# Kernel optimization log

Hardware: AMD Instinct MI355X
Metric: run time of the kernel (lower is better)

## Reference

```python
import jax, jax.numpy as jnp
import numpy as np

N_RES = 320
C_Z = 128
NUM_HEAD = 4
HEAD_DIM = C_Z // NUM_HEAD  # 32
LN_EPS = 1e-5


def layer_norm(x, scale, offset):
    mean = jnp.mean(x, axis=-1, keepdims=True)
    var = jnp.var(x, axis=-1, keepdims=True)
    return (x - mean) * jax.lax.rsqrt(var + LN_EPS) * scale + offset


def setup_inputs() -> dict:
    key = jax.random.key(0)
    ks = jax.random.split(key, 12)
    d = {
        'pair_act': jax.random.normal(ks[0], (N_RES, N_RES, C_Z), jnp.float32),
        'affine_act': jax.random.normal(ks[1], (N_RES, N_RES, C_Z), jnp.float32),
        'pair_mask': jnp.ones((N_RES, N_RES), jnp.float32),
        'pair_ln_scale': jnp.ones((C_Z,), jnp.float32),
        'pair_ln_offset': jnp.zeros((C_Z,), jnp.float32),
        'affine_ln_scale': jnp.ones((C_Z,), jnp.float32),
        'affine_ln_offset': jnp.zeros((C_Z,), jnp.float32),
        'feat_2d_weights': jax.random.normal(ks[2], (C_Z, NUM_HEAD), jnp.float32) / 0.8796256610342398,
        'query_w': jax.random.normal(ks[3], (C_Z, NUM_HEAD, HEAD_DIM), jnp.float32) * 0.05,
        'key_w': jax.random.normal(ks[4], (C_Z, NUM_HEAD, HEAD_DIM), jnp.float32) * 0.05,
        'value_w': jax.random.normal(ks[5], (C_Z, NUM_HEAD, HEAD_DIM), jnp.float32) * 0.05,
        'gating_w': jax.random.normal(ks[6], (C_Z, NUM_HEAD, HEAD_DIM), jnp.float32) * 0.05,
        'output_w': jax.random.normal(ks[7], (NUM_HEAD, HEAD_DIM, C_Z), jnp.float32) * 0.05,
    }
    return d


def reference(pair_act, affine_act, pair_mask,
              pair_ln_scale, pair_ln_offset, affine_ln_scale, affine_ln_offset,
              feat_2d_weights, query_w, key_w, value_w, gating_w, output_w):
    # orientation == 'per_row' -> no swapaxes
    pair_ln = layer_norm(pair_act, pair_ln_scale, pair_ln_offset)          # [N,N,c]
    affine_ln = layer_norm(affine_act, affine_ln_scale, affine_ln_offset)  # [N,N,c]

    # padding bias [N,1,1,N]
    bias = (1e9 * (pair_mask - 1.0))[:, None, None, :]
    # nonbatched pair bias [H,N,N]
    nonbatched_bias = jnp.einsum('qkc,ch->hqk', affine_ln, feat_2d_weights)

    # attention (q_data == m_data == pair_ln)
    scale = HEAD_DIM ** (-0.5)
    q = jnp.einsum('bqa,ahc->bqhc', pair_ln, query_w) * scale
    k = jnp.einsum('bka,ahc->bkhc', pair_ln, key_w)
    v = jnp.einsum('bka,ahc->bkhc', pair_ln, value_w)

    logits = jnp.einsum('bqhc,bkhc->bhqk', q, k) + bias + nonbatched_bias[None]
    weights = jax.nn.softmax(logits, axis=-1)
    weighted_avg = jnp.einsum('bhqk,bkhc->bqhc', weights, v)

    gate = jax.nn.sigmoid(jnp.einsum('bqc,chv->bqhv', pair_ln, gating_w))
    weighted_avg = weighted_avg * gate

    out = jnp.einsum('bqhc,hco->bqo', weighted_avg, output_w)  # [N,N,c_z]
    return out
```

## Files before the change

### kernel.cpp

```cpp
#include <hip/hip_runtime.h>
#include <hip/hip_bf16.h>

#define N_RES 320
#define C_Z   128
#define NH    4
#define HD    32
#define M_TOT (N_RES*N_RES)
#define LN_EPS 1e-5f
#define QSCALE 0.17677669529663687f

typedef __attribute__((ext_vector_type(8))) short short8;
typedef __attribute__((ext_vector_type(4))) float floatx4;

typedef const __hip_bfloat16* bfp;

__device__ __forceinline__ float lo_bits(unsigned u){
    union { unsigned u; float f; } v; v.u = u << 16; return v.f;
}
__device__ __forceinline__ float hi_bits(unsigned u){
    union { unsigned u; float f; } v; v.u = u & 0xffff0000u; return v.f;
}
__device__ __forceinline__ float u16_to_f(unsigned short s){
    union { unsigned u; float f; } v; v.u = ((unsigned)s) << 16; return v.f;
}
__device__ __forceinline__ unsigned short bf16r(float f){
    union { __hip_bfloat16 b; unsigned short s; } v; v.b = __float2bfloat16(f); return v.s;
}
__device__ __forceinline__ unsigned pack2(float a, float b){
    return (unsigned)bf16r(a) | ((unsigned)bf16r(b) << 16);
}
__device__ __forceinline__ float wave_sum(float x){
    #pragma unroll
    for (int off = 32; off > 0; off >>= 1) x += __shfl_xor(x, off, 64);
    return x;
}

__device__ __forceinline__ short8 gather_w(const unsigned short* __restrict__ wm,
                                           int h, int ctc, int ks, int quad){
    short8 f;
    #pragma unroll
    for (int j = 0; j < 8; ++j)
        f[j] = (short)wm[(ks*32 + quad*8 + j)*128 + h*32 + ctc];
    return f;
}

__global__ __launch_bounds__(256) void k_conv_all(
    const void* __restrict__ s_mask, const void* __restrict__ s_pls,
    const void* __restrict__ s_plo,  const void* __restrict__ s_als,
    const void* __restrict__ s_alo,  const void* __restrict__ s_fw,
    const void* __restrict__ s_wq,   const void* __restrict__ s_wk,
    const void* __restrict__ s_wv,   const void* __restrict__ s_wg,
    const void* __restrict__ s_wo,
    unsigned short* __restrict__ arena, const unsigned* __restrict__ probe)
{
    int gid = blockIdx.x * 256 + threadIdx.x;
    const void* src; int off;
    if      (gid < 102400){ src = s_mask; off = gid; }
    else if (gid < 102528){ src = s_pls;  off = gid - 102400; }
    else if (gid < 102656){ src = s_plo;  off = gid - 102528; }
    else if (gid < 102784){ src = s_als;  off = gid - 102656; }
    else if (gid < 102912){ src = s_alo;  off = gid - 102784; }
    else if (gid < 103424){ src = s_fw;   off = gid - 102912; }
    else if (gid < 119808){ src = s_wq;   off = gid - 103424; }
    else if (gid < 136192){ src = s_wk;   off = gid - 119808; }
    else if (gid < 152576){ src = s_wv;   off = gid - 136192; }
    else if (gid < 168960){ src = s_wg;   off = gid - 152576; }
    else                  { src = s_wo;   off = gid - 168960; }
    if (probe[0] & 0xffffu)
        arena[gid] = ((const unsigned short*)src)[off];
    else
        arena[gid] = bf16r(((const float*)src)[off]);
}

__global__ __launch_bounds__(256) void k_affine_ln_nb(
    const void* __restrict__ affine,
    const unsigned short* __restrict__ sc, const unsigned short* __restrict__ of,
    const unsigned short* __restrict__ fw, float* __restrict__ nb,
    const unsigned* __restrict__ probe)
{
    int wave = threadIdx.x >> 6, lane = threadIdx.x & 63;
    int row = blockIdx.x * 4 + wave;
    float x0, x1;
    if (probe[0] & 0xffffu){
        unsigned u = ((const unsigned*)affine)[(size_t)row * 64 + lane];
        x0 = lo_bits(u); x1 = hi_bits(u);
    } else {
        float2 f = ((const float2*)affine)[(size_t)row * 64 + lane];
        x0 = f.x; x1 = f.y;
    }
    float s  = wave_sum(x0 + x1);
    float ss = wave_sum(x0*x0 + x1*x1);
    float mean = s * (1.0f/128.0f);
    float var  = ss * (1.0f/128.0f) - mean*mean;
    float rs   = rsqrtf(var + LN_EPS);
    float ln0 = (x0 - mean) * rs * u16_to_f(sc[2*lane])   + u16_to_f(of[2*lane]);
    float ln1 = (x1 - mean) * rs * u16_to_f(sc[2*lane+1]) + u16_to_f(of[2*lane+1]);
    #pragma unroll
    for (int hh = 0; hh < NH; ++hh){
        float p = ln0 * u16_to_f(fw[(2*lane)*NH + hh])
                + ln1 * u16_to_f(fw[(2*lane+1)*NH + hh]);
        p = wave_sum(p);
        if (lane == 0) nb[(size_t)hh * M_TOT + row] = p;
    }
}

__global__ __launch_bounds__(256) void k_pair_ln(
    const void* __restrict__ pair,
    const unsigned short* __restrict__ sc, const unsigned short* __restrict__ of,
    unsigned* __restrict__ pl, const unsigned* __restrict__ probe)
{
    int wave = threadIdx.x >> 6, lane = threadIdx.x & 63;
    int row = blockIdx.x * 4 + wave;
    float x0, x1;
    if (probe[0] & 0xffffu){
        unsigned u = ((const unsigned*)pair)[(size_t)row * 64 + lane];
        x0 = lo_bits(u); x1 = hi_bits(u);
    } else {
        float2 f = ((const float2*)pair)[(size_t)row * 64 + lane];
        x0 = f.x; x1 = f.y;
    }
    float s  = wave_sum(x0 + x1);
    float ss = wave_sum(x0*x0 + x1*x1);
    float mean = s * (1.0f/128.0f);
    float var  = ss * (1.0f/128.0f) - mean*mean;
    float rs   = rsqrtf(var + LN_EPS);
    float ln0 = (x0 - mean) * rs * u16_to_f(sc[2*lane])   + u16_to_f(of[2*lane]);
    float ln1 = (x1 - mean) * rs * u16_to_f(sc[2*lane+1]) + u16_to_f(of[2*lane+1]);
    pl[(size_t)row * 64 + lane] = pack2(ln0, ln1);
}

__global__ __launch_bounds__(512, 4) void k_attn(
    const unsigned short* __restrict__ pl,
    const unsigned short* __restrict__ wq, const unsigned short* __restrict__ wk,
    const unsigned short* __restrict__ wv, const unsigned short* __restrict__ wg,
    const unsigned short* __restrict__ maskc, const float* __restrict__ nb,
    unsigned short* __restrict__ wab)
{
    __shared__ unsigned short Ks[320*40];
    __shared__ unsigned short Vt[32*328];
    __shared__ unsigned short Pbuf[8*16*40];
    __shared__ float biasl[320];

    int b = blockIdx.x, h = blockIdx.y;
    int tid = threadIdx.x, lane = tid & 63, wave = tid >> 6;
    int c16 = lane & 15, quad = lane >> 4, rb = quad * 4;

    const unsigned short* plrow = pl + (size_t)b * N_RES * C_Z;
    const short8* plrow8 = (const short8*)plrow;
    const short8* Ks8 = (const short8*)Ks;
    const short8* Vt8 = (const short8*)Vt;
    unsigned short* Pw = Pbuf + wave * 640;
    const short8* Pb8 = (const short8*)Pw;

    floatx4 Z = {0.f, 0.f, 0.f, 0.f};
    short8 onesf;
    #pragma unroll
    for (int j = 0; j < 8; ++j) onesf[j] = (short)0x3F80;

    if (tid < 320)
        biasl[tid] = 1e9f * (u16_to_f(maskc[(size_t)b * N_RES + tid]) - 1.0f);

    {
        int mat = wave >> 2, ct = (wave >> 1) & 1, mh = wave & 1;
        const unsigned short* wm = mat ? wv : wk;
        short8 bw[4];
        #pragma unroll
        for (int ks = 0; ks < 4; ++ks) bw[ks] = gather_w(wm, h, ct*16 + c16, ks, quad);
        #pragma unroll 1
        for (int t = 0; t < 10; ++t){
            int mt = mh * 10 + t;
            short8 a[4];
            #pragma unroll
            for (int ks = 0; ks < 4; ++ks)
                a[ks] = plrow8[(mt*16 + c16)*16 + ks*4 + quad];
            floatx4 acc = Z;
            if (mat == 0){
                #pragma unroll
                for (int ks = 0; ks < 4; ++ks)
                    acc = __builtin_amdgcn_mfma_f32_16x16x32_bf16(a[ks], bw[ks], acc, 0, 0, 0);
                #pragma unroll
                for (int i = 0; i < 4; ++i)
                    Ks[(mt*16 + rb + i)*40 + ct*16 + c16] = bf16r(acc[i]);
            } else {
                #pragma unroll
                for (int ks = 0; ks < 4; ++ks)
                    acc = __builtin_amdgcn_mfma_f32_16x16x32_bf16(bw[ks], a[ks], acc, 0, 0, 0);
                #pragma unroll
                for (int i = 0; i < 4; ++i)
                    Vt[(ct*16 + rb + i)*328 + mt*16 + c16] = bf16r(acc[i]);
            }
        }
    }
    __syncthreads();

    const float* nbh = nb + (size_t)h * M_TOT;

    #pragma unroll 1
    for (int mt = wave; mt < 20; mt += 8){
        int m0 = mt * 16;
        floatx4 q0 = Z, q1 = Z;
        #pragma unroll
        for (int ks = 0; ks < 4; ++ks){
            short8 af = plrow8[(m0 + c16)*16 + ks*4 + quad];
            short8 b0 = gather_w(wq, h, c16,      ks, quad);
            short8 b1 = gather_w(wq, h, 16 + c16, ks, quad);
            q0 = __builtin_amdgcn_mfma_f32_16x16x32_bf16(af, b0, q0, 0, 0, 0);
            q1 = __builtin_amdgcn_mfma_f32_16x16x32_bf16(af, b1, q1, 0, 0, 0);
        }
        #pragma unroll
        for (int i = 0; i < 4; ++i){
            Pw[(rb+i)*40 + c16]      = bf16r(q0[i] * QSCALE);
            Pw[(rb+i)*40 + 16 + c16] = bf16r(q1[i] * QSCALE);
        }
        short8 qf = Pb8[c16*5 + quad];

        float m[4]; floatx4 accl = Z, acc0 = Z, acc1 = Z;
        #pragma unroll
        for (int i = 0; i < 4; ++i) m[i] = -3.0e38f;
        int rowbase = (m0 + rb) * N_RES;

        #pragma unroll 1
        for (int kt2 = 0; kt2 < 10; ++kt2){
            int cola = kt2*32 + c16;
            float nba[4], nbb[4];
            #pragma unroll
            for (int i = 0; i < 4; ++i){
                nba[i] = nbh[rowbase + i*N_RES + cola];
                nbb[i] = nbh[rowbase + i*N_RES + cola + 16];
            }
            float ba = biasl[cola], bb = biasl[cola + 16];
            short8 kfa = Ks8[cola*5 + quad];
            short8 kfb = Ks8[(cola+16)*5 + quad];
            floatx4 sa = __builtin_amdgcn_mfma_f32_16x16x32_bf16(qf, kfa, Z, 0, 0, 0);
            floatx4 sb = __builtin_amdgcn_mfma_f32_16x16x32_bf16(qf, kfb, Z, 0, 0, 0);
            float tm[4];
            #pragma unroll
            for (int i = 0; i < 4; ++i){
                sa[i] += ba + nba[i];
                sb[i] += bb + nbb[i];
                tm[i] = fmaxf(sa[i], sb[i]);
            }
            #pragma unroll
            for (int off = 1; off < 16; off <<= 1){
                #pragma unroll
                for (int i = 0; i < 4; ++i)
                    tm[i] = fmaxf(tm[i], __shfl_xor(tm[i], off, 64));
            }
            float al[4];
            #pragma unroll
            for (int i = 0; i < 4; ++i){
                float mn = fmaxf(m[i], tm[i]);
                al[i] = __expf(m[i] - mn);
                m[i] = mn;
                float pa = __expf(sa[i] - mn);
                float pb = __expf(sb[i] - mn);
                Pw[(rb+i)*40 + c16]      = bf16r(pa);
                Pw[(rb+i)*40 + 16 + c16] = bf16r(pb);
                accl[i] *= al[i]; acc0[i] *= al[i]; acc1[i] *= al[i];
            }
            short8 pf = Pb8[c16*5 + quad];
            short8 v0 = Vt8[c16*41      + kt2*4 + quad];
            short8 v1 = Vt8[(c16+16)*41 + kt2*4 + quad];
            accl = __builtin_amdgcn_mfma_f32_16x16x32_bf16(pf, onesf, accl, 0, 0, 0);
            acc0 = __builtin_amdgcn_mfma_f32_16x16x32_bf16(pf, v0, acc0, 0, 0, 0);
            acc1 = __builtin_amdgcn_mfma_f32_16x16x32_bf16(pf, v1, acc1, 0, 0, 0);
        }

        floatx4 g0 = Z, g1 = Z;
        #pragma unroll
        for (int ks = 0; ks < 4; ++ks){
            short8 af = plrow8[(m0 + c16)*16 + ks*4 + quad];
            short8 b0 = gather_w(wg, h, c16,      ks, quad);
            short8 b1 = gather_w(wg, h, 16 + c16, ks, quad);
            g0 = __builtin_amdgcn_mfma_f32_16x16x32_bf16(af, b0, g0, 0, 0, 0);
            g1 = __builtin_amdgcn_mfma_f32_16x16x32_bf16(af, b1, g1, 0, 0, 0);
        }
        #pragma unroll
        for (int i = 0; i < 4; ++i){
            float inv = 1.0f / accl[i];
            float o0 = acc0[i] * inv * (1.0f/(1.0f + __expf(-g0[i])));
            float o1 = acc1[i] * inv * (1.0f/(1.0f + __expf(-g1[i])));
            size_t orow = ((size_t)(b*N_RES + m0 + rb + i))*C_Z + h*HD;
            wab[orow + c16]      = bf16r(o0);
            wab[orow + 16 + c16] = bf16r(o1);
        }
    }
}

__global__ __launch_bounds__(256, 4) void k_outproj(
    const unsigned short* __restrict__ wab, const unsigned short* __restrict__ wo,
    void* __restrict__ out, const unsigned* __restrict__ probe)
{
    __shared__ unsigned short Wot[128*136];
    int tid = threadIdx.x, lane = tid & 63, wave = tid >> 6;
    int c16 = lane & 15, quad = lane >> 4, rb = quad * 4;

    for (int i = tid; i < 16384; i += 256){
        int o = i & 127, z = i >> 7;
        Wot[o*136 + z] = wo[z*128 + o];
    }
    __syncthreads();

    const short8* wab8 = (const short8*)wab;
    const short8* Wot8 = (const short8*)Wot;
    floatx4 Z = {0.f, 0.f, 0.f, 0.f};

    int m0 = blockIdx.x * 64 + wave * 16;
    short8 a[4];
    #pragma unroll
    for (int ks = 0; ks < 4; ++ks)
        a[ks] = wab8[(size_t)(m0 + c16)*16 + ks*4 + quad];

    bool isbf = (probe[0] & 0xffffu) != 0;
    #pragma unroll 1
    for (int nt = 0; nt < 8; ++nt){
        floatx4 acc = Z;
        #pragma unroll
        for (int ks = 0; ks < 4; ++ks){
            short8 bf = Wot8[(nt*16 + c16)*17 + ks*4 + quad];
            acc = __builtin_amdgcn_mfma_f32_16x16x32_bf16(a[ks], bf, acc, 0, 0, 0);
        }
        #pragma unroll
        for (int i = 0; i < 4; ++i){
            size_t idx = (size_t)(m0 + rb + i)*C_Z + nt*16 + c16;
            if (isbf) ((unsigned short*)out)[idx] = bf16r(acc[i]);
            else      ((float*)out)[idx] = acc[i];
        }
    }
}

extern "C" void kernel_launch(void* const* d_in, const int* in_sizes, int n_in,
                              void* d_out, int out_size, void* d_ws, size_t ws_size,
                              hipStream_t stream)
{
    const unsigned* probe = (const unsigned*)d_in[3];

    char* w = (char*)d_ws;
    unsigned short* arena = (unsigned short*)w;
    unsigned short* mask_c = arena + 0;
    unsigned short* pls_c  = arena + 102400;
    unsigned short* plo_c  = arena + 102528;
    unsigned short* als_c  = arena + 102656;
    unsigned short* alo_c  = arena + 102784;
    unsigned short* fw_c   = arena + 102912;
    unsigned short* wq_c   = arena + 103424;
    unsigned short* wk_c   = arena + 119808;
    unsigned short* wv_c   = arena + 136192;
    unsigned short* wg_c   = arena + 152576;
    unsigned short* wo_c   = arena + 168960;
    float*          nb     = (float*)(w + 524288);
    unsigned short* pl     = (unsigned short*)(w + 2162688);
    unsigned short* wab    = (unsigned short*)(w + 28377088);

    k_conv_all<<<724, 256, 0, stream>>>(d_in[2], d_in[3], d_in[4], d_in[5], d_in[6],
                                        d_in[7], d_in[8], d_in[9], d_in[10], d_in[11],
                                        d_in[12], arena, probe);
    k_affine_ln_nb<<<25600, 256, 0, stream>>>(d_in[1], als_c, alo_c, fw_c, nb, probe);
    k_pair_ln    <<<25600, 256, 0, stream>>>(d_in[0], pls_c, plo_c, (unsigned*)pl, probe);
    k_attn       <<<dim3(N_RES, NH), 512, 0, stream>>>(pl, wq_c, wk_c, wv_c, wg_c,
                                                       mask_c, nb, wab);
    k_outproj    <<<1600, 256, 0, stream>>>(wab, wo_c, d_out, probe);
}
```

Measured before the change: 428.8 us.

## Pre-transpose weights, vectorize LN kernels, and restructure attention softmax layout

```diff
diff --git a/kernel.cpp b/kernel.cpp
--- a/kernel.cpp
+++ b/kernel.cpp
@@ -12,14 +12,19 @@
 typedef __attribute__((ext_vector_type(8))) short short8;
 typedef __attribute__((ext_vector_type(4))) float floatx4;
 
-typedef const __hip_bfloat16* bfp;
-
-__device__ __forceinline__ float lo_bits(unsigned u){
-    union { unsigned u; float f; } v; v.u = u << 16; return v.f;
-}
-__device__ __forceinline__ float hi_bits(unsigned u){
-    union { unsigned u; float f; } v; v.u = u & 0xffff0000u; return v.f;
-}
+#define OFF_MASK 0
+#define OFF_PLS  102400
+#define OFF_PLO  102528
+#define OFF_ALS  102656
+#define OFF_ALO  102784
+#define OFF_FWT  102912
+#define OFF_WQT  104960
+#define OFF_WKT  121344
+#define OFF_WVT  137728
+#define OFF_WGT  154112
+#define OFF_WOT  170496
+#define ARENA_N  186880
+
 __device__ __forceinline__ float u16_to_f(unsigned short s){
     union { unsigned u; float f; } v; v.u = ((unsigned)s) << 16; return v.f;
 }
@@ -29,19 +34,8 @@
 __device__ __forceinline__ unsigned pack2(float a, float b){
     return (unsigned)bf16r(a) | ((unsigned)bf16r(b) << 16);
 }
-__device__ __forceinline__ float wave_sum(float x){
-    #pragma unroll
-    for (int off = 32; off > 0; off >>= 1) x += __shfl_xor(x, off, 64);
-    return x;
-}
-
-__device__ __forceinline__ short8 gather_w(const unsigned short* __restrict__ wm,
-                                           int h, int ctc, int ks, int quad){
-    short8 f;
-    #pragma unroll
-    for (int j = 0; j < 8; ++j)
-        f[j] = (short)wm[(ks*32 + quad*8 + j)*128 + h*32 + ctc];
-    return f;
+__device__ __forceinline__ float ld_dual(const void* s, size_t i, bool isbf){
+    return isbf ? u16_to_f(((const unsigned short*)s)[i]) : ((const float*)s)[i];
 }
 
 __global__ __launch_bounds__(256) void k_conv_all(
@@ -54,214 +48,284 @@
     unsigned short* __restrict__ arena, const unsigned* __restrict__ probe)
 {
     int gid = blockIdx.x * 256 + threadIdx.x;
-    const void* src; int off;
-    if      (gid < 102400){ src = s_mask; off = gid; }
-    else if (gid < 102528){ src = s_pls;  off = gid - 102400; }
-    else if (gid < 102656){ src = s_plo;  off = gid - 102528; }
-    else if (gid < 102784){ src = s_als;  off = gid - 102656; }
-    else if (gid < 102912){ src = s_alo;  off = gid - 102784; }
-    else if (gid < 103424){ src = s_fw;   off = gid - 102912; }
-    else if (gid < 119808){ src = s_wq;   off = gid - 103424; }
-    else if (gid < 136192){ src = s_wk;   off = gid - 119808; }
-    else if (gid < 152576){ src = s_wv;   off = gid - 136192; }
-    else if (gid < 168960){ src = s_wg;   off = gid - 152576; }
-    else                  { src = s_wo;   off = gid - 168960; }
-    if (probe[0] & 0xffffu)
-        arena[gid] = ((const unsigned short*)src)[off];
-    else
-        arena[gid] = bf16r(((const float*)src)[off]);
+    bool isbf = (probe[0] & 0xffffu) != 0;
+    float val;
+    if (gid < OFF_PLS)      val = ld_dual(s_mask, gid, isbf);
+    else if (gid < OFF_PLO) val = ld_dual(s_pls, gid - OFF_PLS, isbf);
+    else if (gid < OFF_ALS) val = ld_dual(s_plo, gid - OFF_PLO, isbf);
+    else if (gid < OFF_ALO) val = ld_dual(s_als, gid - OFF_ALS, isbf);
+    else if (gid < OFF_FWT) val = ld_dual(s_alo, gid - OFF_ALO, isbf);
+    else if (gid < OFF_WQT){
+        int local = gid - OFF_FWT, hh = local >> 7, c = local & 127;
+        val = (hh < 4) ? ld_dual(s_fw, c*NH + hh, isbf) : 0.0f;
+    } else if (gid < OFF_WOT){
+        int seg = (gid - OFF_WQT) >> 14;
+        int local = (gid - OFF_WQT) & 16383;
+        int hc = local >> 7, z = local & 127;
+        const void* src = (seg == 0) ? s_wq : (seg == 1) ? s_wk : (seg == 2) ? s_wv : s_wg;
+        val = ld_dual(src, z*128 + hc, isbf);
+    } else {
+        int local = gid - OFF_WOT, o = local >> 7, hc = local & 127;
+        val = ld_dual(s_wo, hc*128 + o, isbf);
+    }
+    arena[gid] = bf16r(val);
 }
 
 __global__ __launch_bounds__(256) void k_affine_ln_nb(
     const void* __restrict__ affine,
     const unsigned short* __restrict__ sc, const unsigned short* __restrict__ of,
-    const unsigned short* __restrict__ fw, float* __restrict__ nb,
+    const unsigned short* __restrict__ fwpT, float* __restrict__ nb,
     const unsigned* __restrict__ probe)
 {
-    int wave = threadIdx.x >> 6, lane = threadIdx.x & 63;
-    int row = blockIdx.x * 4 + wave;
-    float x0, x1;
-    if (probe[0] & 0xffffu){
-        unsigned u = ((const unsigned*)affine)[(size_t)row * 64 + lane];
-        x0 = lo_bits(u); x1 = hi_bits(u);
+    int tid = threadIdx.x, lane = tid & 63, wave = tid >> 6;
+    int c16 = lane & 15, quad = lane >> 4, rb = quad * 4;
+    int m0 = blockIdx.x * 64 + wave * 16;
+    bool isbf = (probe[0] & 0xffffu) != 0;
+
+    float x[32];
+    if (isbf){
+        const short8* a8 = (const short8*)affine;
+        #pragma unroll
+        for (int ks = 0; ks < 4; ++ks){
+            short8 t = a8[(size_t)(m0 + c16)*16 + ks*4 + quad];
+            #pragma unroll
+            for (int j = 0; j < 8; ++j) x[ks*8+j] = u16_to_f((unsigned short)t[j]);
+        }
     } else {
-        float2 f = ((const float2*)affine)[(size_t)row * 64 + lane];
-        x0 = f.x; x1 = f.y;
-    }
-    float s  = wave_sum(x0 + x1);
-    float ss = wave_sum(x0*x0 + x1*x1);
+        const floatx4* a4 = (const floatx4*)affine;
+        #pragma unroll
+        for (int ks = 0; ks < 4; ++ks){
+            floatx4 f0 = a4[(size_t)(m0 + c16)*32 + ks*8 + quad*2];
+            floatx4 f1 = a4[(size_t)(m0 + c16)*32 + ks*8 + quad*2 + 1];
+            #pragma unroll
+            for (int j = 0; j < 4; ++j){ x[ks*8+j] = f0[j]; x[ks*8+4+j] = f1[j]; }
+        }
+    }
+    float s = 0.f, ss = 0.f;
+    #pragma unroll
+    for (int j = 0; j < 32; ++j){ s += x[j]; ss += x[j]*x[j]; }
+    s  += __shfl_xor(s, 16, 64);  s  += __shfl_xor(s, 32, 64);
+    ss += __shfl_xor(ss, 16, 64); ss += __shfl_xor(ss, 32, 64);
     float mean = s * (1.0f/128.0f);
     float var  = ss * (1.0f/128.0f) - mean*mean;
     float rs   = rsqrtf(var + LN_EPS);
-    float ln0 = (x0 - mean) * rs * u16_to_f(sc[2*lane])   + u16_to_f(of[2*lane]);
-    float ln1 = (x1 - mean) * rs * u16_to_f(sc[2*lane+1]) + u16_to_f(of[2*lane+1]);
-    #pragma unroll
-    for (int hh = 0; hh < NH; ++hh){
-        float p = ln0 * u16_to_f(fw[(2*lane)*NH + hh])
-                + ln1 * u16_to_f(fw[(2*lane+1)*NH + hh]);
-        p = wave_sum(p);
-        if (lane == 0) nb[(size_t)hh * M_TOT + row] = p;
-    }
+
+    const short8* sc8 = (const short8*)sc;
+    const short8* of8 = (const short8*)of;
+    short8 lf[4], lg[4];
+    #pragma unroll
+    for (int ks = 0; ks < 4; ++ks){
+        short8 scv = sc8[ks*4 + quad], ofv = of8[ks*4 + quad];
+        #pragma unroll
+        for (int j = 0; j < 8; ++j){
+            float l = (x[ks*8+j] - mean) * rs * u16_to_f((unsigned short)scv[j])
+                    + u16_to_f((unsigned short)ofv[j]);
+            unsigned short hi = bf16r(l);
+            lf[ks][j] = (short)hi;
+            lg[ks][j] = (short)bf16r(l - u16_to_f(hi));
+        }
+    }
+    floatx4 acc = {0.f, 0.f, 0.f, 0.f};
+    const short8* fw8 = (const short8*)fwpT;
+    #pragma unroll
+    for (int ks = 0; ks < 4; ++ks){
+        short8 fwf = fw8[c16*16 + ks*4 + quad];
+        acc = __builtin_amdgcn_mfma_f32_16x16x32_bf16(lf[ks], fwf, acc, 0, 0, 0);
+        acc = __builtin_amdgcn_mfma_f32_16x16x32_bf16(lg[ks], fwf, acc, 0, 0, 0);
+    }
+    if (c16 < 4)
+        *(floatx4*)&nb[(size_t)c16 * M_TOT + m0 + rb] = acc;
 }
 
 __global__ __launch_bounds__(256) void k_pair_ln(
     const void* __restrict__ pair,
     const unsigned short* __restrict__ sc, const unsigned short* __restrict__ of,
-    unsigned* __restrict__ pl, const unsigned* __restrict__ probe)
-{
-    int wave = threadIdx.x >> 6, lane = threadIdx.x & 63;
-    int row = blockIdx.x * 4 + wave;
-    float x0, x1;
-    if (probe[0] & 0xffffu){
-        unsigned u = ((const unsigned*)pair)[(size_t)row * 64 + lane];
-        x0 = lo_bits(u); x1 = hi_bits(u);
+    unsigned short* __restrict__ pl, const unsigned* __restrict__ probe)
+{
+    int tid = threadIdx.x, lane = tid & 63, wave = tid >> 6;
+    int c16 = lane & 15, quad = lane >> 4;
+    int m0 = blockIdx.x * 64 + wave * 16;
+    bool isbf = (probe[0] & 0xffffu) != 0;
+
+    float x[32];
+    if (isbf){
+        const short8* a8 = (const short8*)pair;
+        #pragma unroll
+        for (int ks = 0; ks < 4; ++ks){
+            short8 t = a8[(size_t)(m0 + c16)*16 + ks*4 + quad];
+            #pragma unroll
+            for (int j = 0; j < 8; ++j) x[ks*8+j] = u16_to_f((unsigned short)t[j]);
+        }
     } else {
-        float2 f = ((const float2*)pair)[(size_t)row * 64 + lane];
-        x0 = f.x; x1 = f.y;
-    }
-    float s  = wave_sum(x0 + x1);
-    float ss = wave_sum(x0*x0 + x1*x1);
+        const floatx4* a4 = (const floatx4*)pair;
+        #pragma unroll
+        for (int ks = 0; ks < 4; ++ks){
+            floatx4 f0 = a4[(size_t)(m0 + c16)*32 + ks*8 + quad*2];
+            floatx4 f1 = a4[(size_t)(m0 + c16)*32 + ks*8 + quad*2 + 1];
+            #pragma unroll
+            for (int j = 0; j < 4; ++j){ x[ks*8+j] = f0[j]; x[ks*8+4+j] = f1[j]; }
+        }
+    }
+    float s = 0.f, ss = 0.f;
+    #pragma unroll
+    for (int j = 0; j < 32; ++j){ s += x[j]; ss += x[j]*x[j]; }
+    s  += __shfl_xor(s, 16, 64);  s  += __shfl_xor(s, 32, 64);
+    ss += __shfl_xor(ss, 16, 64); ss += __shfl_xor(ss, 32, 64);
     float mean = s * (1.0f/128.0f);
     float var  = ss * (1.0f/128.0f) - mean*mean;
     float rs   = rsqrtf(var + LN_EPS);
-    float ln0 = (x0 - mean) * rs * u16_to_f(sc[2*lane])   + u16_to_f(of[2*lane]);
-    float ln1 = (x1 - mean) * rs * u16_to_f(sc[2*lane+1]) + u16_to_f(of[2*lane+1]);
-    pl[(size_t)row * 64 + lane] = pack2(ln0, ln1);
+
+    const short8* sc8 = (const short8*)sc;
+    const short8* of8 = (const short8*)of;
+    short8* pl8 = (short8*)pl;
+    #pragma unroll
+    for (int ks = 0; ks < 4; ++ks){
+        short8 scv = sc8[ks*4 + quad], ofv = of8[ks*4 + quad];
+        short8 lf;
+        #pragma unroll
+        for (int j = 0; j < 8; ++j){
+            float l = (x[ks*8+j] - mean) * rs * u16_to_f((unsigned short)scv[j])
+                    + u16_to_f((unsigned short)ofv[j]);
+            lf[j] = (short)bf16r(l);
+        }
+        pl8[(size_t)(m0 + c16)*16 + ks*4 + quad] = lf;
+    }
 }
 
 __global__ __launch_bounds__(512, 4) void k_attn(
     const unsigned short* __restrict__ pl,
-    const unsigned short* __restrict__ wq, const unsigned short* __restrict__ wk,
-    const unsigned short* __restrict__ wv, const unsigned short* __restrict__ wg,
+    const unsigned short* __restrict__ wqT, const unsigned short* __restrict__ wkT,
+    const unsigned short* __restrict__ wvT, const unsigned short* __restrict__ wgT,
     const unsigned short* __restrict__ maskc, const float* __restrict__ nb,
     unsigned short* __restrict__ wab)
 {
-    __shared__ unsigned short Ks[320*40];
-    __shared__ unsigned short Vt[32*328];
-    __shared__ unsigned short Pbuf[8*16*40];
-    __shared__ float biasl[320];
+    __shared__ __align__(16) unsigned short Ks[320*40];
+    __shared__ __align__(16) unsigned short Vt[32*328];
+    __shared__ __align__(16) unsigned short Pbuf[8*640];
+    __shared__ __align__(16) float biasl[320];
 
     int b = blockIdx.x, h = blockIdx.y;
     int tid = threadIdx.x, lane = tid & 63, wave = tid >> 6;
     int c16 = lane & 15, quad = lane >> 4, rb = quad * 4;
 
-    const unsigned short* plrow = pl + (size_t)b * N_RES * C_Z;
-    const short8* plrow8 = (const short8*)plrow;
+    const short8* plrow8 = (const short8*)(pl + (size_t)b * N_RES * C_Z);
     const short8* Ks8 = (const short8*)Ks;
     const short8* Vt8 = (const short8*)Vt;
+    const short8* wqT8 = (const short8*)wqT;
+    const short8* wgT8 = (const short8*)wgT;
     unsigned short* Pw = Pbuf + wave * 640;
     const short8* Pb8 = (const short8*)Pw;
-
     floatx4 Z = {0.f, 0.f, 0.f, 0.f};
-    short8 onesf;
-    #pragma unroll
-    for (int j = 0; j < 8; ++j) onesf[j] = (short)0x3F80;
 
     if (tid < 320)
         biasl[tid] = 1e9f * (u16_to_f(maskc[(size_t)b * N_RES + tid]) - 1.0f);
 
-    {
-        int mat = wave >> 2, ct = (wave >> 1) & 1, mh = wave & 1;
-        const unsigned short* wm = mat ? wv : wk;
-        short8 bw[4];
-        #pragma unroll
-        for (int ks = 0; ks < 4; ++ks) bw[ks] = gather_w(wm, h, ct*16 + c16, ks, quad);
-        #pragma unroll 1
-        for (int t = 0; t < 10; ++t){
-            int mt = mh * 10 + t;
-            short8 a[4];
+    #pragma unroll 1
+    for (int t = wave; t < 80; t += 8){
+        int isV = (t >= 40) ? 1 : 0;
+        int r = isV ? t - 40 : t;
+        int ct = (r >= 20) ? 1 : 0;
+        int mt = (r >= 20) ? r - 20 : r;
+        int hc = h*HD + ct*16 + c16;
+        const short8* WT8 = (const short8*)(isV ? wvT : wkT);
+        short8 bw[4], a[4];
+        #pragma unroll
+        for (int ks = 0; ks < 4; ++ks){
+            bw[ks] = WT8[hc*16 + ks*4 + quad];
+            a[ks]  = plrow8[(mt*16 + c16)*16 + ks*4 + quad];
+        }
+        floatx4 acc = Z;
+        if (!isV){
             #pragma unroll
             for (int ks = 0; ks < 4; ++ks)
-                a[ks] = plrow8[(mt*16 + c16)*16 + ks*4 + quad];
-            floatx4 acc = Z;
-            if (mat == 0){
-                #pragma unroll
-                for (int ks = 0; ks < 4; ++ks)
-                    acc = __builtin_amdgcn_mfma_f32_16x16x32_bf16(a[ks], bw[ks], acc, 0, 0, 0);
-                #pragma unroll
-                for (int i = 0; i < 4; ++i)
-                    Ks[(mt*16 + rb + i)*40 + ct*16 + c16] = bf16r(acc[i]);
-            } else {
-                #pragma unroll
-                for (int ks = 0; ks < 4; ++ks)
-                    acc = __builtin_amdgcn_mfma_f32_16x16x32_bf16(bw[ks], a[ks], acc, 0, 0, 0);
-                #pragma unroll
-                for (int i = 0; i < 4; ++i)
-                    Vt[(ct*16 + rb + i)*328 + mt*16 + c16] = bf16r(acc[i]);
-            }
+                acc = __builtin_amdgcn_mfma_f32_16x16x32_bf16(a[ks], bw[ks], acc, 0, 0, 0);
+            #pragma unroll
+            for (int i = 0; i < 4; ++i)
+                Ks[(mt*16 + rb + i)*40 + ct*16 + c16] = bf16r(acc[i]);
+        } else {
+            #pragma unroll
+            for (int ks = 0; ks < 4; ++ks)
+                acc = __builtin_amdgcn_mfma_f32_16x16x32_bf16(bw[ks], a[ks], acc, 0, 0, 0);
+            #pragma unroll
+            for (int i = 0; i < 4; ++i)
+                Vt[(ct*16 + rb + i)*328 + mt*16 + c16] = bf16r(acc[i]);
         }
     }
     __syncthreads();
-
-    const float* nbh = nb + (size_t)h * M_TOT;
 
     #pragma unroll 1
     for (int mt = wave; mt < 20; mt += 8){
         int m0 = mt * 16;
+        short8 plf[4];
+        #pragma unroll
+        for (int ks = 0; ks < 4; ++ks)
+            plf[ks] = plrow8[(m0 + c16)*16 + ks*4 + quad];
+
         floatx4 q0 = Z, q1 = Z;
         #pragma unroll
         for (int ks = 0; ks < 4; ++ks){
-            short8 af = plrow8[(m0 + c16)*16 + ks*4 + quad];
-            short8 b0 = gather_w(wq, h, c16,      ks, quad);
-            short8 b1 = gather_w(wq, h, 16 + c16, ks, quad);
-            q0 = __builtin_amdgcn_mfma_f32_16x16x32_bf16(af, b0, q0, 0, 0, 0);
-            q1 = __builtin_amdgcn_mfma_f32_16x16x32_bf16(af, b1, q1, 0, 0, 0);
-        }
-        #pragma unroll
-        for (int i = 0; i < 4; ++i){
-            Pw[(rb+i)*40 + c16]      = bf16r(q0[i] * QSCALE);
-            Pw[(rb+i)*40 + 16 + c16] = bf16r(q1[i] * QSCALE);
+            short8 w0 = wqT8[(h*HD + c16)*16 + ks*4 + quad];
+            short8 w1 = wqT8[(h*HD + 16 + c16)*16 + ks*4 + quad];
+            q0 = __builtin_amdgcn_mfma_f32_16x16x32_bf16(w0, plf[ks], q0, 0, 0, 0);
+            q1 = __builtin_amdgcn_mfma_f32_16x16x32_bf16(w1, plf[ks], q1, 0, 0, 0);
+        }
+        {
+            uint2 pk0 = { pack2(q0[0]*QSCALE, q0[1]*QSCALE), pack2(q0[2]*QSCALE, q0[3]*QSCALE) };
+            uint2 pk1 = { pack2(q1[0]*QSCALE, q1[1]*QSCALE), pack2(q1[2]*QSCALE, q1[3]*QSCALE) };
+            *(uint2*)&Pw[c16*40 + quad*4]      = pk0;
+            *(uint2*)&Pw[c16*40 + 16 + quad*4] = pk1;
         }
         short8 qf = Pb8[c16*5 + quad];
 
-        float m[4]; floatx4 accl = Z, acc0 = Z, acc1 = Z;
-        #pragma unroll
-        for (int i = 0; i < 4; ++i) m[i] = -3.0e38f;
-        int rowbase = (m0 + rb) * N_RES;
+        float mrow = -3.0e38f, lrow = 0.f;
+        floatx4 acc0 = Z, acc1 = Z;
+        const float* nbq = nb + (size_t)h * M_TOT + (size_t)(m0 + c16) * N_RES;
 
         #pragma unroll 1
         for (int kt2 = 0; kt2 < 10; ++kt2){
-            int cola = kt2*32 + c16;
-            float nba[4], nbb[4];
+            int k0 = kt2 * 32;
+            short8 kfa = Ks8[(k0 + c16)*5 + quad];
+            short8 kfb = Ks8[(k0 + 16 + c16)*5 + quad];
+            floatx4 sa = __builtin_amdgcn_mfma_f32_16x16x32_bf16(kfa, qf, Z, 0, 0, 0);
+            floatx4 sb = __builtin_amdgcn_mfma_f32_16x16x32_bf16(kfb, qf, Z, 0, 0, 0);
+            floatx4 nba = *(const floatx4*)&nbq[k0 + quad*4];
+            floatx4 nbb = *(const floatx4*)&nbq[k0 + 16 + quad*4];
+            floatx4 bia = *(const floatx4*)&biasl[k0 + quad*4];
+            floatx4 bib = *(const floatx4*)&biasl[k0 + 16 + quad*4];
+            float tm = -3.0e38f;
             #pragma unroll
             for (int i = 0; i < 4; ++i){
-                nba[i] = nbh[rowbase + i*N_RES + cola];
-                nbb[i] = nbh[rowbase + i*N_RES + cola + 16];
+                sa[i] += nba[i] + bia[i];
+                sb[i] += nbb[i] + bib[i];
+                tm = fmaxf(tm, fmaxf(sa[i], sb[i]));
             }
-            float ba = biasl[cola], bb = biasl[cola + 16];
-            short8 kfa = Ks8[cola*5 + quad];
-            short8 kfb = Ks8[(cola+16)*5 + quad];
-            floatx4 sa = __builtin_amdgcn_mfma_f32_16x16x32_bf16(qf, kfa, Z, 0, 0, 0);
-            floatx4 sb = __builtin_amdgcn_mfma_f32_16x16x32_bf16(qf, kfb, Z, 0, 0, 0);
-            float tm[4];
+            tm = fmaxf(tm, __shfl_xor(tm, 16, 64));
+            tm = fmaxf(tm, __shfl_xor(tm, 32, 64));
+            float mn = fmaxf(mrow, tm);
+            float alpha = __expf(mrow - mn);
+            mrow = mn;
+            float pa[4], pb[4], tsum = 0.f;
             #pragma unroll
             for (int i = 0; i < 4; ++i){
-                sa[i] += ba + nba[i];
-                sb[i] += bb + nbb[i];
-                tm[i] = fmaxf(sa[i], sb[i]);
+                pa[i] = __expf(sa[i] - mn);
+                pb[i] = __expf(sb[i] - mn);
+                tsum += pa[i] + pb[i];
             }
-            #pragma unroll
-            for (int off = 1; off < 16; off <<= 1){
-                #pragma unroll
-                for (int i = 0; i < 4; ++i)
-                    tm[i] = fmaxf(tm[i], __shfl_xor(tm[i], off, 64));
+            tsum += __shfl_xor(tsum, 16, 64);
+            tsum += __shfl_xor(tsum, 32, 64);
+            lrow = lrow * alpha + tsum;
+            uint2 wa = { pack2(pa[0], pa[1]), pack2(pa[2], pa[3]) };
+            uint2 wb = { pack2(pb[0], pb[1]), pack2(pb[2], pb[3]) };
+            *(uint2*)&Pw[c16*40 + quad*4]      = wa;
+            *(uint2*)&Pw[c16*40 + 16 + quad*4] = wb;
+            short8 pf = Pb8[c16*5 + quad];
+            short8 v0 = Vt8[c16*41 + kt2*4 + quad];
+            short8 v1 = Vt8[(16 + c16)*41 + kt2*4 + quad];
+            #pragma unroll
+            for (int i = 0; i < 4; ++i){
+                float al = __shfl(alpha, rb + i, 64);
+                acc0[i] *= al; acc1[i] *= al;
             }
-            float al[4];
-            #pragma unroll
-            for (int i = 0; i < 4; ++i){
-                float mn = fmaxf(m[i], tm[i]);
-                al[i] = __expf(m[i] - mn);
-                m[i] = mn;
-                float pa = __expf(sa[i] - mn);
-                float pb = __expf(sb[i] - mn);
-                Pw[(rb+i)*40 + c16]      = bf16r(pa);
-                Pw[(rb+i)*40 + 16 + c16] = bf16r(pb);
-                accl[i] *= al[i]; acc0[i] *= al[i]; acc1[i] *= al[i];
-            }
-            short8 pf = Pb8[c16*5 + quad];
-            short8 v0 = Vt8[c16*41      + kt2*4 + quad];
-            short8 v1 = Vt8[(c16+16)*41 + kt2*4 + quad];
-            accl = __builtin_amdgcn_mfma_f32_16x16x32_bf16(pf, onesf, accl, 0, 0, 0);
             acc0 = __builtin_amdgcn_mfma_f32_16x16x32_bf16(pf, v0, acc0, 0, 0, 0);
             acc1 = __builtin_amdgcn_mfma_f32_16x16x32_bf16(pf, v1, acc1, 0, 0, 0);
         }
@@ -269,18 +333,18 @@
         floatx4 g0 = Z, g1 = Z;
         #pragma unroll
         for (int ks = 0; ks < 4; ++ks){
-            short8 af = plrow8[(m0 + c16)*16 + ks*4 + quad];
-            short8 b0 = gather_w(wg, h, c16,      ks, quad);
-            short8 b1 = gather_w(wg, h, 16 + c16, ks, quad);
-            g0 = __builtin_amdgcn_mfma_f32_16x16x32_bf16(af, b0, g0, 0, 0, 0);
-            g1 = __builtin_amdgcn_mfma_f32_16x16x32_bf16(af, b1, g1, 0, 0, 0);
+            short8 w0 = wgT8[(h*HD + c16)*16 + ks*4 + quad];
+            short8 w1 = wgT8[(h*HD + 16 + c16)*16 + ks*4 + quad];
+            g0 = __builtin_amdgcn_mfma_f32_16x16x32_bf16(plf[ks], w0, g0, 0, 0, 0);
+            g1 = __builtin_amdgcn_mfma_f32_16x16x32_bf16(plf[ks], w1, g1, 0, 0, 0);
         }
         #pragma unroll
         for (int i = 0; i < 4; ++i){
-            float inv = 1.0f / accl[i];
+            float li = __shfl(lrow, rb + i, 64);
+            float inv = 1.0f / li;
             float o0 = acc0[i] * inv * (1.0f/(1.0f + __expf(-g0[i])));
             float o1 = acc1[i] * inv * (1.0f/(1.0f + __expf(-g1[i])));
-            size_t orow = ((size_t)(b*N_RES + m0 + rb + i))*C_Z + h*HD;
+            size_t orow = (size_t)h * (M_TOT*HD) + (size_t)(b*N_RES + m0 + rb + i) * HD;
             wab[orow + c16]      = bf16r(o0);
             wab[orow + 16 + c16] = bf16r(o1);
         }
@@ -288,36 +352,29 @@
 }
 
 __global__ __launch_bounds__(256, 4) void k_outproj(
-    const unsigned short* __restrict__ wab, const unsigned short* __restrict__ wo,
+    const unsigned short* __restrict__ wab, const unsigned short* __restrict__ woT,
     void* __restrict__ out, const unsigned* __restrict__ probe)
 {
-    __shared__ unsigned short Wot[128*136];
     int tid = threadIdx.x, lane = tid & 63, wave = tid >> 6;
     int c16 = lane & 15, quad = lane >> 4, rb = quad * 4;
-
-    for (int i = tid; i < 16384; i += 256){
-        int o = i & 127, z = i >> 7;
-        Wot[o*136 + z] = wo[z*128 + o];
-    }
-    __syncthreads();
+    int m0 = blockIdx.x * 64 + wave * 16;
+    bool isbf = (probe[0] & 0xffffu) != 0;
 
     const short8* wab8 = (const short8*)wab;
-    const short8* Wot8 = (const short8*)Wot;
+    const short8* woT8 = (const short8*)woT;
     floatx4 Z = {0.f, 0.f, 0.f, 0.f};
 
-    int m0 = blockIdx.x * 64 + wave * 16;
     short8 a[4];
     #pragma unroll
     for (int ks = 0; ks < 4; ++ks)
-        a[ks] = wab8[(size_t)(m0 + c16)*16 + ks*4 + quad];
-
-    bool isbf = (probe[0] & 0xffffu) != 0;
+        a[ks] = wab8[(size_t)ks * (M_TOT*4) + (size_t)(m0 + c16)*4 + quad];
+
     #pragma unroll 1
     for (int nt = 0; nt < 8; ++nt){
         floatx4 acc = Z;
         #pragma unroll
         for (int ks = 0; ks < 4; ++ks){
-            short8 bf = Wot8[(nt*16 + c16)*17 + ks*4 + quad];
+            short8 bf = woT8[(nt*16 + c16)*16 + ks*4 + quad];
             acc = __builtin_amdgcn_mfma_f32_16x16x32_bf16(a[ks], bf, acc, 0, 0, 0);
         }
         #pragma unroll
@@ -337,27 +394,27 @@
 
     char* w = (char*)d_ws;
     unsigned short* arena = (unsigned short*)w;
-    unsigned short* mask_c = arena + 0;
-    unsigned short* pls_c  = arena + 102400;
-    unsigned short* plo_c  = arena + 102528;
-    unsigned short* als_c  = arena + 102656;
-    unsigned short* alo_c  = arena + 102784;
-    unsigned short* fw_c   = arena + 102912;
-    unsigned short* wq_c   = arena + 103424;
-    unsigned short* wk_c   = arena + 119808;
-    unsigned short* wv_c   = arena + 136192;
-    unsigned short* wg_c   = arena + 152576;
-    unsigned short* wo_c   = arena + 168960;
+    unsigned short* mask_c = arena + OFF_MASK;
+    unsigned short* pls_c  = arena + OFF_PLS;
+    unsigned short* plo_c  = arena + OFF_PLO;
+    unsigned short* als_c  = arena + OFF_ALS;
+    unsigned short* alo_c  = arena + OFF_ALO;
+    unsigned short* fwT_c  = arena + OFF_FWT;
+    unsigned short* wqT_c  = arena + OFF_WQT;
+    unsigned short* wkT_c  = arena + OFF_WKT;
+    unsigned short* wvT_c  = arena + OFF_WVT;
+    unsigned short* wgT_c  = arena + OFF_WGT;
+    unsigned short* woT_c  = arena + OFF_WOT;
     float*          nb     = (float*)(w + 524288);
     unsigned short* pl     = (unsigned short*)(w + 2162688);
     unsigned short* wab    = (unsigned short*)(w + 28377088);
 
-    k_conv_all<<<724, 256, 0, stream>>>(d_in[2], d_in[3], d_in[4], d_in[5], d_in[6],
+    k_conv_all<<<730, 256, 0, stream>>>(d_in[2], d_in[3], d_in[4], d_in[5], d_in[6],
                                         d_in[7], d_in[8], d_in[9], d_in[10], d_in[11],
                                         d_in[12], arena, probe);
-    k_affine_ln_nb<<<25600, 256, 0, stream>>>(d_in[1], als_c, alo_c, fw_c, nb, probe);
-    k_pair_ln    <<<25600, 256, 0, stream>>>(d_in[0], pls_c, plo_c, (unsigned*)pl, probe);
-    k_attn       <<<dim3(N_RES, NH), 512, 0, stream>>>(pl, wq_c, wk_c, wv_c, wg_c,
+    k_affine_ln_nb<<<1600, 256, 0, stream>>>(d_in[1], als_c, alo_c, fwT_c, nb, probe);
+    k_pair_ln    <<<1600, 256, 0, stream>>>(d_in[0], pls_c, plo_c, pl, probe);
+    k_attn       <<<dim3(N_RES, NH), 512, 0, stream>>>(pl, wqT_c, wkT_c, wvT_c, wgT_c,
                                                        mask_c, nb, wab);
-    k_outproj    <<<1600, 256, 0, stream>>>(wab, wo_c, d_out, probe);
-}
+    k_outproj    <<<1600, 256, 0, stream>>>(wab, woT_c, d_out, probe);
+}
```

New measurement: 411.8 us. 1.04x faster.
